# Optimization experiments

Measured on AMD Instinct MI355X. Metric: run time of the kernel, lower is better.

Reference implementation:

```python
import jax, jax.numpy as jnp
import numpy as np

N = 50000
E = 800000
IN_C, HID, OUT_C = 512, 256, 128


def gcn_conv(x, edge_index, W, b, num_nodes):
    # PyG GCNConv: add self-loops, symmetric normalization, linear-then-aggregate.
    h = x @ W  # [N, out]
    src = jnp.concatenate([edge_index[0], jnp.arange(num_nodes)])
    dst = jnp.concatenate([edge_index[1], jnp.arange(num_nodes)])
    ones = jnp.ones(src.shape[0], dtype=x.dtype)
    deg = jax.ops.segment_sum(ones, dst, num_segments=num_nodes)  # in-degree incl. self-loop
    dinv = jax.lax.rsqrt(deg)  # deg >= 1 thanks to self-loops
    norm = dinv[src] * dinv[dst]  # [E+N]
    msg = h[src] * norm[:, None]  # gather + scale
    out = jax.ops.segment_sum(msg, dst, num_segments=num_nodes)  # scatter-add
    return out + b


def setup_inputs() -> dict:
    key = jax.random.key(0)
    k_x, k_e, k_w1, k_b1, k_w2, k_b2 = jax.random.split(key, 6)
    x = jax.random.normal(k_x, (N, IN_C), dtype=jnp.float32)
    edge_index = jax.random.randint(k_e, (2, E), 0, N, dtype=jnp.int64)
    s1 = 1.0 / np.sqrt(IN_C)
    s2 = 1.0 / np.sqrt(HID)
    W1 = jax.random.uniform(k_w1, (IN_C, HID), jnp.float32, -s1, s1)
    b1 = jax.random.uniform(k_b1, (HID,), jnp.float32, -s1, s1)
    W2 = jax.random.uniform(k_w2, (HID, OUT_C), jnp.float32, -s2, s2)
    b2 = jax.random.uniform(k_b2, (OUT_C,), jnp.float32, -s2, s2)
    return {"x": x, "edge_index": edge_index, "W1": W1, "b1": b1, "W2": W2, "b2": b2}


def reference(x, edge_index, W1, b1, W2, b2):
    h = gcn_conv(x, edge_index, W1, b1, N)
    h = jax.nn.relu(h)
    # dropout in eval mode == identity
    return gcn_conv(h, edge_index, W2, b2, N)
```

## Files before the change

### kernel.cpp

```cpp
#include <hip/hip_runtime.h>
#include <stdint.h>

typedef __bf16 bf16_t;
typedef bf16_t bf16x8 __attribute__((ext_vector_type(8)));
typedef bf16_t bf16x4 __attribute__((ext_vector_type(4)));
typedef bf16_t bf16x2 __attribute__((ext_vector_type(2)));
typedef float  f32x4  __attribute__((ext_vector_type(4)));

#define IN_C 512
#define HID  256
#define OUTC 128

__global__ void k_detect(const void* __restrict__ ei, int* __restrict__ flag, int n_nodes) {
  if (blockIdx.x == 0 && threadIdx.x == 0) {
    const long long* p = (const long long*)ei;
    int ok = 1;
    for (int i = 0; i < 64; ++i) {
      long long v = p[i];
      if (v < 0 || v >= n_nodes) ok = 0;
    }
    *flag = ok;
  }
}

__global__ void k_decode_hist(const void* __restrict__ ei, const int* __restrict__ flag,
                              int* __restrict__ srcI, int* __restrict__ dstI,
                              int* __restrict__ cnt, int E) {
  int e = blockIdx.x * blockDim.x + threadIdx.x;
  if (e >= E) return;
  int s, d;
  if (*flag) {
    const long long* p = (const long long*)ei;
    s = (int)p[e];
    d = (int)p[(size_t)E + e];
  } else {
    const int* p = (const int*)ei;
    s = p[e];
    d = p[E + e];
  }
  srcI[e] = s;
  dstI[e] = d;
  atomicAdd(&cnt[d], 1);
}

__global__ void k_dinv(const int* __restrict__ cnt, float* __restrict__ dinv, int n) {
  int i = blockIdx.x * blockDim.x + threadIdx.x;
  if (i < n) dinv[i] = rsqrtf((float)cnt[i] + 1.0f);
}

__global__ void k_scan1(const int* __restrict__ cnt, int* __restrict__ ex,
                        int* __restrict__ part, int n) {
  __shared__ int sh[256];
  int i = blockIdx.x * 256 + threadIdx.x;
  int v = (i < n) ? cnt[i] : 0;
  sh[threadIdx.x] = v;
  __syncthreads();
  int val = v;
  for (int off = 1; off < 256; off <<= 1) {
    int t = (threadIdx.x >= off) ? sh[threadIdx.x - off] : 0;
    __syncthreads();
    val += t;
    sh[threadIdx.x] = val;
    __syncthreads();
  }
  if (i < n) ex[i] = val - v;
  if (threadIdx.x == 255) part[blockIdx.x] = val;
}

__global__ void k_scan2(int* __restrict__ part, int nb) {
  __shared__ int sh[256];
  int v = (threadIdx.x < nb) ? part[threadIdx.x] : 0;
  sh[threadIdx.x] = v;
  __syncthreads();
  int val = v;
  for (int off = 1; off < 256; off <<= 1) {
    int t = (threadIdx.x >= off) ? sh[threadIdx.x - off] : 0;
    __syncthreads();
    val += t;
    sh[threadIdx.x] = val;
    __syncthreads();
  }
  if (threadIdx.x < nb) part[threadIdx.x] = val - v;
}

__global__ void k_scan3(int* __restrict__ rs, const int* __restrict__ part,
                        int* __restrict__ cur, int n, int Etot) {
  int i = blockIdx.x * 256 + threadIdx.x;
  if (i < n) {
    int r = rs[i] + part[blockIdx.x];
    rs[i] = r;
    cur[i] = r;
  }
  if (i == 0) rs[n] = Etot;
}

__global__ void k_fill(const int* __restrict__ srcI, const int* __restrict__ dstI,
                       int* __restrict__ cur, int* __restrict__ csr, int E) {
  int e = blockIdx.x * blockDim.x + threadIdx.x;
  if (e >= E) return;
  int p = atomicAdd(&cur[dstI[e]], 1);
  csr[p] = srcI[e];
}

__global__ void k_convx(const float* __restrict__ x, bf16_t* __restrict__ Xb,
                        int n, int mpad) {
  int t = blockIdx.x * blockDim.x + threadIdx.x;
  int r = t >> 6, c8 = t & 63;
  if (r >= mpad) return;
  bf16x8 o;
  if (r < n) {
    const float4* px = (const float4*)(x + (size_t)r * IN_C);
    float4 a = px[c8 * 2];
    float4 b = px[c8 * 2 + 1];
    o[0] = (bf16_t)a.x; o[1] = (bf16_t)a.y; o[2] = (bf16_t)a.z; o[3] = (bf16_t)a.w;
    o[4] = (bf16_t)b.x; o[5] = (bf16_t)b.y; o[6] = (bf16_t)b.z; o[7] = (bf16_t)b.w;
  } else {
    for (int i = 0; i < 8; ++i) o[i] = (bf16_t)0.0f;
  }
  *(bf16x8*)(Xb + (size_t)r * IN_C + c8 * 8) = o;
}

__global__ void k_transpose(const float* __restrict__ W, bf16_t* __restrict__ Wt,
                            int K, int Ncols) {
  int t = blockIdx.x * blockDim.x + threadIdx.x;
  if (t >= K * Ncols) return;
  int k = t / Ncols, nn = t % Ncols;
  Wt[(size_t)nn * K + k] = (bf16_t)W[t];
}

__global__ __launch_bounds__(256, 2) void k_gemm(const bf16_t* __restrict__ A,
                                                 const bf16_t* __restrict__ Bt,
                                                 bf16_t* __restrict__ C,
                                                 int Kdim, int Ncols) {
  __shared__ bf16_t As[128 * 40];
  __shared__ bf16_t Bs[128 * 40];
  const int bm = blockIdx.x, bn = blockIdx.y;
  const int tid = threadIdx.x;
  const int wave = tid >> 6, lane = tid & 63;
  const int wm = (wave >> 1) * 64, wn = (wave & 1) * 64;
  const int quad = lane >> 4, l16 = lane & 15;
  const int seg = tid & 3;

  f32x4 acc[4][4];
  for (int i = 0; i < 4; ++i)
    for (int j = 0; j < 4; ++j)
      for (int r = 0; r < 4; ++r) acc[i][j][r] = 0.0f;

  for (int kk = 0; kk < Kdim; kk += 32) {
#pragma unroll
    for (int s = 0; s < 2; ++s) {
      int row = s * 64 + (tid >> 2);
      bf16x8 va = *(const bf16x8*)(A + (size_t)(bm * 128 + row) * Kdim + kk + seg * 8);
      *(bf16x8*)(&As[row * 40 + seg * 8]) = va;
      bf16x8 vb = *(const bf16x8*)(Bt + (size_t)(bn * 128 + row) * Kdim + kk + seg * 8);
      *(bf16x8*)(&Bs[row * 40 + seg * 8]) = vb;
    }
    __syncthreads();
    bf16x8 af[4], bfr[4];
#pragma unroll
    for (int i = 0; i < 4; ++i)
      af[i] = *(const bf16x8*)(&As[(wm + i * 16 + l16) * 40 + quad * 8]);
#pragma unroll
    for (int j = 0; j < 4; ++j)
      bfr[j] = *(const bf16x8*)(&Bs[(wn + j * 16 + l16) * 40 + quad * 8]);
#pragma unroll
    for (int i = 0; i < 4; ++i)
#pragma unroll
      for (int j = 0; j < 4; ++j)
        acc[i][j] = __builtin_amdgcn_mfma_f32_16x16x32_bf16(af[i], bfr[j], acc[i][j], 0, 0, 0);
    __syncthreads();
  }

#pragma unroll
  for (int i = 0; i < 4; ++i) {
#pragma unroll
    for (int j = 0; j < 4; ++j) {
      int col = bn * 128 + wn + j * 16 + l16;
      int row0 = bm * 128 + wm + i * 16 + quad * 4;
#pragma unroll
      for (int r = 0; r < 4; ++r)
        C[(size_t)(row0 + r) * Ncols + col] = (bf16_t)acc[i][j][r];
    }
  }
}

__global__ void k_agg_l1(const bf16_t* __restrict__ H, const int* __restrict__ rs,
                         const int* __restrict__ csr, const float* __restrict__ dinv,
                         const float* __restrict__ b1, bf16_t* __restrict__ R,
                         int n, int mpad) {
  int d = blockIdx.x * 4 + (threadIdx.x >> 6);
  if (d >= mpad) return;
  int lane = threadIdx.x & 63;
  if (d >= n) {
    bf16x4 z;
    z[0] = (bf16_t)0.0f; z[1] = (bf16_t)0.0f; z[2] = (bf16_t)0.0f; z[3] = (bf16_t)0.0f;
    *(bf16x4*)(R + (size_t)d * HID + lane * 4) = z;
    return;
  }
  int e0 = rs[d], e1 = rs[d + 1];
  float a0 = 0.f, a1 = 0.f, a2 = 0.f, a3 = 0.f;
  float c0 = 0.f, c1 = 0.f, c2 = 0.f, c3 = 0.f;
  int e = e0;
  for (; e + 2 <= e1; e += 2) {
    int s0 = csr[e], s1 = csr[e + 1];
    float w0 = dinv[s0], w1 = dinv[s1];
    bf16x4 h0 = *(const bf16x4*)(H + (size_t)s0 * HID + lane * 4);
    bf16x4 h1 = *(const bf16x4*)(H + (size_t)s1 * HID + lane * 4);
    a0 += w0 * (float)h0[0]; a1 += w0 * (float)h0[1];
    a2 += w0 * (float)h0[2]; a3 += w0 * (float)h0[3];
    c0 += w1 * (float)h1[0]; c1 += w1 * (float)h1[1];
    c2 += w1 * (float)h1[2]; c3 += w1 * (float)h1[3];
  }
  if (e < e1) {
    int s0 = csr[e];
    float w0 = dinv[s0];
    bf16x4 h0 = *(const bf16x4*)(H + (size_t)s0 * HID + lane * 4);
    a0 += w0 * (float)h0[0]; a1 += w0 * (float)h0[1];
    a2 += w0 * (float)h0[2]; a3 += w0 * (float)h0[3];
  }
  a0 += c0; a1 += c1; a2 += c2; a3 += c3;
  float dd = dinv[d];
  float dv2 = dd * dd;
  bf16x4 hs = *(const bf16x4*)(H + (size_t)d * HID + lane * 4);
  float4 bb = ((const float4*)b1)[lane];
  float v0 = fmaxf(a0 * dd + dv2 * (float)hs[0] + bb.x, 0.f);
  float v1 = fmaxf(a1 * dd + dv2 * (float)hs[1] + bb.y, 0.f);
  float v2 = fmaxf(a2 * dd + dv2 * (float)hs[2] + bb.z, 0.f);
  float v3 = fmaxf(a3 * dd + dv2 * (float)hs[3] + bb.w, 0.f);
  bf16x4 o;
  o[0] = (bf16_t)v0; o[1] = (bf16_t)v1; o[2] = (bf16_t)v2; o[3] = (bf16_t)v3;
  *(bf16x4*)(R + (size_t)d * HID + lane * 4) = o;
}

__global__ void k_agg_l2(const bf16_t* __restrict__ H, const int* __restrict__ rs,
                         const int* __restrict__ csr, const float* __restrict__ dinv,
                         const float* __restrict__ b2, float* __restrict__ out, int n) {
  int d = blockIdx.x * 4 + (threadIdx.x >> 6);
  if (d >= n) return;
  int lane = threadIdx.x & 63;
  int e0 = rs[d], e1 = rs[d + 1];
  float a0 = 0.f, a1 = 0.f, c0 = 0.f, c1 = 0.f;
  int e = e0;
  for (; e + 2 <= e1; e += 2) {
    int s0 = csr[e], s1 = csr[e + 1];
    float w0 = dinv[s0], w1 = dinv[s1];
    bf16x2 h0 = *(const bf16x2*)(H + (size_t)s0 * OUTC + lane * 2);
    bf16x2 h1 = *(const bf16x2*)(H + (size_t)s1 * OUTC + lane * 2);
    a0 += w0 * (float)h0[0]; a1 += w0 * (float)h0[1];
    c0 += w1 * (float)h1[0]; c1 += w1 * (float)h1[1];
  }
  if (e < e1) {
    int s0 = csr[e];
    float w0 = dinv[s0];
    bf16x2 h0 = *(const bf16x2*)(H + (size_t)s0 * OUTC + lane * 2);
    a0 += w0 * (float)h0[0]; a1 += w0 * (float)h0[1];
  }
  a0 += c0; a1 += c1;
  float dd = dinv[d];
  float dv2 = dd * dd;
  bf16x2 hs = *(const bf16x2*)(H + (size_t)d * OUTC + lane * 2);
  float2 bb = ((const float2*)b2)[lane];
  float2 o;
  o.x = a0 * dd + dv2 * (float)hs[0] + bb.x;
  o.y = a1 * dd + dv2 * (float)hs[1] + bb.y;
  ((float2*)(out + (size_t)d * OUTC))[lane] = o;
}

extern "C" void kernel_launch(void* const* d_in, const int* in_sizes, int n_in,
                              void* d_out, int out_size, void* d_ws, size_t ws_size,
                              hipStream_t stream) {
  const float* x  = (const float*)d_in[0];
  const void*  ei = d_in[1];
  const float* W1 = (const float*)d_in[2];
  const float* b1 = (const float*)d_in[3];
  const float* W2 = (const float*)d_in[4];
  const float* b2 = (const float*)d_in[5];

  const int n = in_sizes[0] / IN_C;
  const int E = in_sizes[1] / 2;
  const int mpad = (n + 127) & ~127;

  char* w = (char*)d_ws;
  size_t off = 0;
  auto alloc = [&](size_t bytes) -> void* {
    void* p = w + off;
    off = (off + bytes + 255) & ~(size_t)255;
    return p;
  };

  int*    flag = (int*)alloc(4);
  int*    srcI = (int*)alloc((size_t)E * 4);
  int*    dstI = (int*)alloc((size_t)E * 4);
  int*    cnt  = (int*)alloc((size_t)n * 4);
  float*  dinv = (float*)alloc((size_t)n * 4);
  int*    rs   = (int*)alloc((size_t)(n + 1) * 4);
  int*    cur  = (int*)alloc((size_t)n * 4);
  int*    part = (int*)alloc(1024);
  int*    csr  = (int*)alloc((size_t)E * 4);
  bf16_t* Xb   = (bf16_t*)alloc((size_t)mpad * IN_C * 2);
  bf16_t* W1t  = (bf16_t*)alloc((size_t)HID * IN_C * 2);
  bf16_t* H1b  = (bf16_t*)alloc((size_t)mpad * HID * 2);
  bf16_t* R1b  = (bf16_t*)alloc((size_t)mpad * HID * 2);
  bf16_t* W2t  = (bf16_t*)alloc((size_t)OUTC * HID * 2);
  bf16_t* H2b  = (bf16_t*)alloc((size_t)mpad * OUTC * 2);
  (void)ws_size; (void)n_in; (void)out_size;

  const int nb = (n + 255) / 256;

  hipMemsetAsync(cnt, 0, (size_t)n * 4, stream);
  k_detect<<<1, 64, 0, stream>>>(ei, flag, n);
  k_decode_hist<<<(E + 255) / 256, 256, 0, stream>>>(ei, flag, srcI, dstI, cnt, E);
  k_dinv<<<nb, 256, 0, stream>>>(cnt, dinv, n);
  k_scan1<<<nb, 256, 0, stream>>>(cnt, rs, part, n);
  k_scan2<<<1, 256, 0, stream>>>(part, nb);
  k_scan3<<<nb, 256, 0, stream>>>(rs, part, cur, n, E);
  k_fill<<<(E + 255) / 256, 256, 0, stream>>>(srcI, dstI, cur, csr, E);

  k_convx<<<(mpad * 64 + 255) / 256, 256, 0, stream>>>(x, Xb, n, mpad);
  k_transpose<<<(IN_C * HID + 255) / 256, 256, 0, stream>>>(W1, W1t, IN_C, HID);
  k_transpose<<<(HID * OUTC + 255) / 256, 256, 0, stream>>>(W2, W2t, HID, OUTC);

  k_gemm<<<dim3(mpad / 128, HID / 128), 256, 0, stream>>>(Xb, W1t, H1b, IN_C, HID);
  k_agg_l1<<<(mpad + 3) / 4, 256, 0, stream>>>(H1b, rs, csr, dinv, b1, R1b, n, mpad);
  k_gemm<<<dim3(mpad / 128, OUTC / 128), 256, 0, stream>>>(R1b, W2t, H2b, HID, OUTC);
  k_agg_l2<<<(n + 3) / 4, 256, 0, stream>>>(H2b, rs, csr, dinv, b2, (float*)d_out, n);
}
```

Before: 421.7 us.

## Fuse fp32-to-bf16 conversion into GEMM1, merge prep kernels, widen aggregation unroll

GEMM1 now reads fp32 x directly and converts to bf16 while staging tiles, which removes the separate conversion pass and the bf16 copy of x. The GEMM tiles change to 64 rows by the full output width, so GEMM1 uses one column block instead of two and each x tile is read once. Edge decode no longer writes int32 src/dst arrays: the histogram reads dst directly and the fill re-reads the raw edges, dinv is computed inside scan1, and the two weight transposes share one launch. The aggregation loops process four edges per step with independent accumulators to keep more gathers in flight, at the cost of more registers per thread.

```diff
diff --git a/kernel.cpp b/kernel.cpp
--- a/kernel.cpp
+++ b/kernel.cpp
@@ -23,9 +23,65 @@
   }
 }
 
-__global__ void k_decode_hist(const void* __restrict__ ei, const int* __restrict__ flag,
-                              int* __restrict__ srcI, int* __restrict__ dstI,
-                              int* __restrict__ cnt, int E) {
+__global__ void k_hist(const void* __restrict__ ei, const int* __restrict__ flag,
+                       int* __restrict__ cnt, int E) {
+  int e = blockIdx.x * blockDim.x + threadIdx.x;
+  if (e >= E) return;
+  int d;
+  if (*flag) d = (int)((const long long*)ei)[(size_t)E + e];
+  else       d = ((const int*)ei)[E + e];
+  atomicAdd(&cnt[d], 1);
+}
+
+__global__ void k_scan1(const int* __restrict__ cnt, int* __restrict__ ex,
+                        int* __restrict__ part, float* __restrict__ dinv, int n) {
+  __shared__ int sh[256];
+  int i = blockIdx.x * 256 + threadIdx.x;
+  int v = (i < n) ? cnt[i] : 0;
+  if (i < n) dinv[i] = rsqrtf((float)v + 1.0f);
+  sh[threadIdx.x] = v;
+  __syncthreads();
+  int val = v;
+  for (int off = 1; off < 256; off <<= 1) {
+    int t = (threadIdx.x >= off) ? sh[threadIdx.x - off] : 0;
+    __syncthreads();
+    val += t;
+    sh[threadIdx.x] = val;
+    __syncthreads();
+  }
+  if (i < n) ex[i] = val - v;
+  if (threadIdx.x == 255) part[blockIdx.x] = val;
+}
+
+__global__ void k_scan2(int* __restrict__ part, int nb) {
+  __shared__ int sh[256];
+  int v = (threadIdx.x < nb) ? part[threadIdx.x] : 0;
+  sh[threadIdx.x] = v;
+  __syncthreads();
+  int val = v;
+  for (int off = 1; off < 256; off <<= 1) {
+    int t = (threadIdx.x >= off) ? sh[threadIdx.x - off] : 0;
+    __syncthreads();
+    val += t;
+    sh[threadIdx.x] = val;
+    __syncthreads();
+  }
+  if (threadIdx.x < nb) part[threadIdx.x] = val - v;
+}
+
+__global__ void k_scan3(int* __restrict__ rs, const int* __restrict__ part,
+                        int* __restrict__ cur, int n, int Etot) {
+  int i = blockIdx.x * 256 + threadIdx.x;
+  if (i < n) {
+    int r = rs[i] + part[blockIdx.x];
+    rs[i] = r;
+    cur[i] = r;
+  }
+  if (i == 0) rs[n] = Etot;
+}
+
+__global__ void k_fill(const void* __restrict__ ei, const int* __restrict__ flag,
+                       int* __restrict__ cur, int* __restrict__ csr, int E) {
   int e = blockIdx.x * blockDim.x + threadIdx.x;
   if (e >= E) return;
   int s, d;
@@ -38,133 +94,124 @@
     s = p[e];
     d = p[E + e];
   }
-  srcI[e] = s;
-  dstI[e] = d;
-  atomicAdd(&cnt[d], 1);
-}
-
-__global__ void k_dinv(const int* __restrict__ cnt, float* __restrict__ dinv, int n) {
-  int i = blockIdx.x * blockDim.x + threadIdx.x;
-  if (i < n) dinv[i] = rsqrtf((float)cnt[i] + 1.0f);
-}
-
-__global__ void k_scan1(const int* __restrict__ cnt, int* __restrict__ ex,
-                        int* __restrict__ part, int n) {
-  __shared__ int sh[256];
-  int i = blockIdx.x * 256 + threadIdx.x;
-  int v = (i < n) ? cnt[i] : 0;
-  sh[threadIdx.x] = v;
-  __syncthreads();
-  int val = v;
-  for (int off = 1; off < 256; off <<= 1) {
-    int t = (threadIdx.x >= off) ? sh[threadIdx.x - off] : 0;
-    __syncthreads();
-    val += t;
-    sh[threadIdx.x] = val;
-    __syncthreads();
-  }
-  if (i < n) ex[i] = val - v;
-  if (threadIdx.x == 255) part[blockIdx.x] = val;
-}
-
-__global__ void k_scan2(int* __restrict__ part, int nb) {
-  __shared__ int sh[256];
-  int v = (threadIdx.x < nb) ? part[threadIdx.x] : 0;
-  sh[threadIdx.x] = v;
-  __syncthreads();
-  int val = v;
-  for (int off = 1; off < 256; off <<= 1) {
-    int t = (threadIdx.x >= off) ? sh[threadIdx.x - off] : 0;
-    __syncthreads();
-    val += t;
-    sh[threadIdx.x] = val;
-    __syncthreads();
-  }
-  if (threadIdx.x < nb) part[threadIdx.x] = val - v;
-}
-
-__global__ void k_scan3(int* __restrict__ rs, const int* __restrict__ part,
-                        int* __restrict__ cur, int n, int Etot) {
-  int i = blockIdx.x * 256 + threadIdx.x;
-  if (i < n) {
-    int r = rs[i] + part[blockIdx.x];
-    rs[i] = r;
-    cur[i] = r;
-  }
-  if (i == 0) rs[n] = Etot;
-}
-
-__global__ void k_fill(const int* __restrict__ srcI, const int* __restrict__ dstI,
-                       int* __restrict__ cur, int* __restrict__ csr, int E) {
-  int e = blockIdx.x * blockDim.x + threadIdx.x;
-  if (e >= E) return;
-  int p = atomicAdd(&cur[dstI[e]], 1);
-  csr[p] = srcI[e];
-}
-
-__global__ void k_convx(const float* __restrict__ x, bf16_t* __restrict__ Xb,
-                        int n, int mpad) {
+  int pos = atomicAdd(&cur[d], 1);
+  csr[pos] = s;
+}
+
+__global__ void k_transw(const float* __restrict__ W1, const float* __restrict__ W2,
+                         bf16_t* __restrict__ W1t, bf16_t* __restrict__ W2t) {
   int t = blockIdx.x * blockDim.x + threadIdx.x;
-  int r = t >> 6, c8 = t & 63;
-  if (r >= mpad) return;
-  bf16x8 o;
-  if (r < n) {
-    const float4* px = (const float4*)(x + (size_t)r * IN_C);
-    float4 a = px[c8 * 2];
-    float4 b = px[c8 * 2 + 1];
-    o[0] = (bf16_t)a.x; o[1] = (bf16_t)a.y; o[2] = (bf16_t)a.z; o[3] = (bf16_t)a.w;
-    o[4] = (bf16_t)b.x; o[5] = (bf16_t)b.y; o[6] = (bf16_t)b.z; o[7] = (bf16_t)b.w;
+  if (t < IN_C * HID) {
+    int k = t / HID, nn = t % HID;
+    W1t[(size_t)nn * IN_C + k] = (bf16_t)W1[t];
   } else {
-    for (int i = 0; i < 8; ++i) o[i] = (bf16_t)0.0f;
-  }
-  *(bf16x8*)(Xb + (size_t)r * IN_C + c8 * 8) = o;
-}
-
-__global__ void k_transpose(const float* __restrict__ W, bf16_t* __restrict__ Wt,
-                            int K, int Ncols) {
-  int t = blockIdx.x * blockDim.x + threadIdx.x;
-  if (t >= K * Ncols) return;
-  int k = t / Ncols, nn = t % Ncols;
-  Wt[(size_t)nn * K + k] = (bf16_t)W[t];
-}
-
-__global__ __launch_bounds__(256, 2) void k_gemm(const bf16_t* __restrict__ A,
-                                                 const bf16_t* __restrict__ Bt,
-                                                 bf16_t* __restrict__ C,
-                                                 int Kdim, int Ncols) {
-  __shared__ bf16_t As[128 * 40];
-  __shared__ bf16_t Bs[128 * 40];
-  const int bm = blockIdx.x, bn = blockIdx.y;
+    int u = t - IN_C * HID;
+    if (u < HID * OUTC) {
+      int k = u / OUTC, nn = u % OUTC;
+      W2t[(size_t)nn * HID + k] = (bf16_t)W2[u];
+    }
+  }
+}
+
+__global__ __launch_bounds__(256, 2) void k_gemm1(const float* __restrict__ x,
+                                                  const bf16_t* __restrict__ Bt,
+                                                  bf16_t* __restrict__ C, int n) {
+  __shared__ bf16_t As[64 * 40];
+  __shared__ bf16_t Bs[256 * 40];
+  const int bm = blockIdx.x;
   const int tid = threadIdx.x;
   const int wave = tid >> 6, lane = tid & 63;
-  const int wm = (wave >> 1) * 64, wn = (wave & 1) * 64;
+  const int wm = (wave >> 1) * 32, wn = (wave & 1) * 128;
   const int quad = lane >> 4, l16 = lane & 15;
-  const int seg = tid & 3;
-
-  f32x4 acc[4][4];
-  for (int i = 0; i < 4; ++i)
+  const int arow = tid >> 2, acol = (tid & 3) * 8;
+  const int grow = bm * 64 + arow;
+
+  f32x4 acc[2][8];
+  for (int i = 0; i < 2; ++i)
+    for (int j = 0; j < 8; ++j)
+      for (int r = 0; r < 4; ++r) acc[i][j][r] = 0.0f;
+
+  for (int kk = 0; kk < IN_C; kk += 32) {
+    bf16x8 va;
+    if (grow < n) {
+      const float4* px = (const float4*)(x + (size_t)grow * IN_C + kk + acol);
+      float4 a = px[0], b = px[1];
+      va[0] = (bf16_t)a.x; va[1] = (bf16_t)a.y; va[2] = (bf16_t)a.z; va[3] = (bf16_t)a.w;
+      va[4] = (bf16_t)b.x; va[5] = (bf16_t)b.y; va[6] = (bf16_t)b.z; va[7] = (bf16_t)b.w;
+    } else {
+      for (int i = 0; i < 8; ++i) va[i] = (bf16_t)0.0f;
+    }
+    *(bf16x8*)(&As[arow * 40 + acol]) = va;
+#pragma unroll
+    for (int c = 0; c < 4; ++c) {
+      bf16x8 vb = *(const bf16x8*)(Bt + (size_t)tid * IN_C + kk + c * 8);
+      *(bf16x8*)(&Bs[tid * 40 + c * 8]) = vb;
+    }
+    __syncthreads();
+    bf16x8 af[2], bfr[8];
+#pragma unroll
+    for (int i = 0; i < 2; ++i)
+      af[i] = *(const bf16x8*)(&As[(wm + i * 16 + l16) * 40 + quad * 8]);
+#pragma unroll
+    for (int j = 0; j < 8; ++j)
+      bfr[j] = *(const bf16x8*)(&Bs[(wn + j * 16 + l16) * 40 + quad * 8]);
+#pragma unroll
+    for (int i = 0; i < 2; ++i)
+#pragma unroll
+      for (int j = 0; j < 8; ++j)
+        acc[i][j] = __builtin_amdgcn_mfma_f32_16x16x32_bf16(af[i], bfr[j], acc[i][j], 0, 0, 0);
+    __syncthreads();
+  }
+
+#pragma unroll
+  for (int i = 0; i < 2; ++i) {
+#pragma unroll
+    for (int j = 0; j < 8; ++j) {
+      int col = wn + j * 16 + l16;
+      int row0 = bm * 64 + wm + i * 16 + quad * 4;
+#pragma unroll
+      for (int r = 0; r < 4; ++r)
+        C[(size_t)(row0 + r) * HID + col] = (bf16_t)acc[i][j][r];
+    }
+  }
+}
+
+__global__ __launch_bounds__(256, 2) void k_gemm2(const bf16_t* __restrict__ A,
+                                                  const bf16_t* __restrict__ Bt,
+                                                  bf16_t* __restrict__ C) {
+  __shared__ bf16_t As[64 * 40];
+  __shared__ bf16_t Bs[128 * 40];
+  const int bm = blockIdx.x;
+  const int tid = threadIdx.x;
+  const int wave = tid >> 6, lane = tid & 63;
+  const int wm = (wave >> 1) * 32, wn = (wave & 1) * 64;
+  const int quad = lane >> 4, l16 = lane & 15;
+  const int arow = tid >> 2, acol = (tid & 3) * 8;
+  const int brow = tid >> 1, bcol = (tid & 1) * 16;
+
+  f32x4 acc[2][4];
+  for (int i = 0; i < 2; ++i)
     for (int j = 0; j < 4; ++j)
       for (int r = 0; r < 4; ++r) acc[i][j][r] = 0.0f;
 
-  for (int kk = 0; kk < Kdim; kk += 32) {
-#pragma unroll
-    for (int s = 0; s < 2; ++s) {
-      int row = s * 64 + (tid >> 2);
-      bf16x8 va = *(const bf16x8*)(A + (size_t)(bm * 128 + row) * Kdim + kk + seg * 8);
-      *(bf16x8*)(&As[row * 40 + seg * 8]) = va;
-      bf16x8 vb = *(const bf16x8*)(Bt + (size_t)(bn * 128 + row) * Kdim + kk + seg * 8);
-      *(bf16x8*)(&Bs[row * 40 + seg * 8]) = vb;
-    }
-    __syncthreads();
-    bf16x8 af[4], bfr[4];
-#pragma unroll
-    for (int i = 0; i < 4; ++i)
+  for (int kk = 0; kk < HID; kk += 32) {
+    bf16x8 va = *(const bf16x8*)(A + (size_t)(bm * 64 + arow) * HID + kk + acol);
+    *(bf16x8*)(&As[arow * 40 + acol]) = va;
+#pragma unroll
+    for (int c = 0; c < 2; ++c) {
+      bf16x8 vb = *(const bf16x8*)(Bt + (size_t)brow * HID + kk + bcol + c * 8);
+      *(bf16x8*)(&Bs[brow * 40 + bcol + c * 8]) = vb;
+    }
+    __syncthreads();
+    bf16x8 af[2], bfr[4];
+#pragma unroll
+    for (int i = 0; i < 2; ++i)
       af[i] = *(const bf16x8*)(&As[(wm + i * 16 + l16) * 40 + quad * 8]);
 #pragma unroll
     for (int j = 0; j < 4; ++j)
       bfr[j] = *(const bf16x8*)(&Bs[(wn + j * 16 + l16) * 40 + quad * 8]);
 #pragma unroll
-    for (int i = 0; i < 4; ++i)
+    for (int i = 0; i < 2; ++i)
 #pragma unroll
       for (int j = 0; j < 4; ++j)
         acc[i][j] = __builtin_amdgcn_mfma_f32_16x16x32_bf16(af[i], bfr[j], acc[i][j], 0, 0, 0);
@@ -172,14 +219,14 @@
   }
 
 #pragma unroll
-  for (int i = 0; i < 4; ++i) {
+  for (int i = 0; i < 2; ++i) {
 #pragma unroll
     for (int j = 0; j < 4; ++j) {
-      int col = bn * 128 + wn + j * 16 + l16;
-      int row0 = bm * 128 + wm + i * 16 + quad * 4;
+      int col = wn + j * 16 + l16;
+      int row0 = bm * 64 + wm + i * 16 + quad * 4;
 #pragma unroll
       for (int r = 0; r < 4; ++r)
-        C[(size_t)(row0 + r) * Ncols + col] = (bf16_t)acc[i][j][r];
+        C[(size_t)(row0 + r) * OUTC + col] = (bf16_t)acc[i][j][r];
     }
   }
 }
@@ -198,31 +245,40 @@
     return;
   }
   int e0 = rs[d], e1 = rs[d + 1];
-  float a0 = 0.f, a1 = 0.f, a2 = 0.f, a3 = 0.f;
-  float c0 = 0.f, c1 = 0.f, c2 = 0.f, c3 = 0.f;
+  float acc[4][4];
+  for (int k = 0; k < 4; ++k)
+    for (int c = 0; c < 4; ++c) acc[k][c] = 0.f;
   int e = e0;
-  for (; e + 2 <= e1; e += 2) {
-    int s0 = csr[e], s1 = csr[e + 1];
-    float w0 = dinv[s0], w1 = dinv[s1];
+  for (; e + 4 <= e1; e += 4) {
+    int s0 = csr[e], s1 = csr[e + 1], s2 = csr[e + 2], s3 = csr[e + 3];
+    float w0 = dinv[s0], w1 = dinv[s1], w2 = dinv[s2], w3 = dinv[s3];
     bf16x4 h0 = *(const bf16x4*)(H + (size_t)s0 * HID + lane * 4);
     bf16x4 h1 = *(const bf16x4*)(H + (size_t)s1 * HID + lane * 4);
-    a0 += w0 * (float)h0[0]; a1 += w0 * (float)h0[1];
-    a2 += w0 * (float)h0[2]; a3 += w0 * (float)h0[3];
-    c0 += w1 * (float)h1[0]; c1 += w1 * (float)h1[1];
-    c2 += w1 * (float)h1[2]; c3 += w1 * (float)h1[3];
-  }
-  if (e < e1) {
+    bf16x4 h2 = *(const bf16x4*)(H + (size_t)s2 * HID + lane * 4);
+    bf16x4 h3 = *(const bf16x4*)(H + (size_t)s3 * HID + lane * 4);
+#pragma unroll
+    for (int c = 0; c < 4; ++c) {
+      acc[0][c] += w0 * (float)h0[c];
+      acc[1][c] += w1 * (float)h1[c];
+      acc[2][c] += w2 * (float)h2[c];
+      acc[3][c] += w3 * (float)h3[c];
+    }
+  }
+  for (; e < e1; ++e) {
     int s0 = csr[e];
     float w0 = dinv[s0];
     bf16x4 h0 = *(const bf16x4*)(H + (size_t)s0 * HID + lane * 4);
-    a0 += w0 * (float)h0[0]; a1 += w0 * (float)h0[1];
-    a2 += w0 * (float)h0[2]; a3 += w0 * (float)h0[3];
-  }
-  a0 += c0; a1 += c1; a2 += c2; a3 += c3;
+#pragma unroll
+    for (int c = 0; c < 4; ++c) acc[0][c] += w0 * (float)h0[c];
+  }
   float dd = dinv[d];
   float dv2 = dd * dd;
   bf16x4 hs = *(const bf16x4*)(H + (size_t)d * HID + lane * 4);
   float4 bb = ((const float4*)b1)[lane];
+  float a0 = acc[0][0] + acc[1][0] + acc[2][0] + acc[3][0];
+  float a1 = acc[0][1] + acc[1][1] + acc[2][1] + acc[3][1];
+  float a2 = acc[0][2] + acc[1][2] + acc[2][2] + acc[3][2];
+  float a3 = acc[0][3] + acc[1][3] + acc[2][3] + acc[3][3];
   float v0 = fmaxf(a0 * dd + dv2 * (float)hs[0] + bb.x, 0.f);
   float v1 = fmaxf(a1 * dd + dv2 * (float)hs[1] + bb.y, 0.f);
   float v2 = fmaxf(a2 * dd + dv2 * (float)hs[2] + bb.z, 0.f);
@@ -239,23 +295,29 @@
   if (d >= n) return;
   int lane = threadIdx.x & 63;
   int e0 = rs[d], e1 = rs[d + 1];
-  float a0 = 0.f, a1 = 0.f, c0 = 0.f, c1 = 0.f;
+  float acc[4][2];
+  for (int k = 0; k < 4; ++k) { acc[k][0] = 0.f; acc[k][1] = 0.f; }
   int e = e0;
-  for (; e + 2 <= e1; e += 2) {
-    int s0 = csr[e], s1 = csr[e + 1];
-    float w0 = dinv[s0], w1 = dinv[s1];
+  for (; e + 4 <= e1; e += 4) {
+    int s0 = csr[e], s1 = csr[e + 1], s2 = csr[e + 2], s3 = csr[e + 3];
+    float w0 = dinv[s0], w1 = dinv[s1], w2 = dinv[s2], w3 = dinv[s3];
     bf16x2 h0 = *(const bf16x2*)(H + (size_t)s0 * OUTC + lane * 2);
     bf16x2 h1 = *(const bf16x2*)(H + (size_t)s1 * OUTC + lane * 2);
-    a0 += w0 * (float)h0[0]; a1 += w0 * (float)h0[1];
-    c0 += w1 * (float)h1[0]; c1 += w1 * (float)h1[1];
-  }
-  if (e < e1) {
+    bf16x2 h2 = *(const bf16x2*)(H + (size_t)s2 * OUTC + lane * 2);
+    bf16x2 h3 = *(const bf16x2*)(H + (size_t)s3 * OUTC + lane * 2);
+    acc[0][0] += w0 * (float)h0[0]; acc[0][1] += w0 * (float)h0[1];
+    acc[1][0] += w1 * (float)h1[0]; acc[1][1] += w1 * (float)h1[1];
+    acc[2][0] += w2 * (float)h2[0]; acc[2][1] += w2 * (float)h2[1];
+    acc[3][0] += w3 * (float)h3[0]; acc[3][1] += w3 * (float)h3[1];
+  }
+  for (; e < e1; ++e) {
     int s0 = csr[e];
     float w0 = dinv[s0];
     bf16x2 h0 = *(const bf16x2*)(H + (size_t)s0 * OUTC + lane * 2);
-    a0 += w0 * (float)h0[0]; a1 += w0 * (float)h0[1];
-  }
-  a0 += c0; a1 += c1;
+    acc[0][0] += w0 * (float)h0[0]; acc[0][1] += w0 * (float)h0[1];
+  }
+  float a0 = acc[0][0] + acc[1][0] + acc[2][0] + acc[3][0];
+  float a1 = acc[0][1] + acc[1][1] + acc[2][1] + acc[3][1];
   float dd = dinv[d];
   float dv2 = dd * dd;
   bf16x2 hs = *(const bf16x2*)(H + (size_t)d * OUTC + lane * 2);
@@ -278,7 +340,7 @@
 
   const int n = in_sizes[0] / IN_C;
   const int E = in_sizes[1] / 2;
-  const int mpad = (n + 127) & ~127;
+  const int mpad = (n + 63) & ~63;
 
   char* w = (char*)d_ws;
   size_t off = 0;
@@ -289,19 +351,16 @@
   };
 
   int*    flag = (int*)alloc(4);
-  int*    srcI = (int*)alloc((size_t)E * 4);
-  int*    dstI = (int*)alloc((size_t)E * 4);
   int*    cnt  = (int*)alloc((size_t)n * 4);
   float*  dinv = (float*)alloc((size_t)n * 4);
   int*    rs   = (int*)alloc((size_t)(n + 1) * 4);
   int*    cur  = (int*)alloc((size_t)n * 4);
   int*    part = (int*)alloc(1024);
   int*    csr  = (int*)alloc((size_t)E * 4);
-  bf16_t* Xb   = (bf16_t*)alloc((size_t)mpad * IN_C * 2);
   bf16_t* W1t  = (bf16_t*)alloc((size_t)HID * IN_C * 2);
+  bf16_t* W2t  = (bf16_t*)alloc((size_t)OUTC * HID * 2);
   bf16_t* H1b  = (bf16_t*)alloc((size_t)mpad * HID * 2);
   bf16_t* R1b  = (bf16_t*)alloc((size_t)mpad * HID * 2);
-  bf16_t* W2t  = (bf16_t*)alloc((size_t)OUTC * HID * 2);
   bf16_t* H2b  = (bf16_t*)alloc((size_t)mpad * OUTC * 2);
   (void)ws_size; (void)n_in; (void)out_size;
 
@@ -309,19 +368,15 @@
 
   hipMemsetAsync(cnt, 0, (size_t)n * 4, stream);
   k_detect<<<1, 64, 0, stream>>>(ei, flag, n);
-  k_decode_hist<<<(E + 255) / 256, 256, 0, stream>>>(ei, flag, srcI, dstI, cnt, E);
-  k_dinv<<<nb, 256, 0, stream>>>(cnt, dinv, n);
-  k_scan1<<<nb, 256, 0, stream>>>(cnt, rs, part, n);
+  k_hist<<<(E + 255) / 256, 256, 0, stream>>>(ei, flag, cnt, E);
+  k_scan1<<<nb, 256, 0, stream>>>(cnt, rs, part, dinv, n);
   k_scan2<<<1, 256, 0, stream>>>(part, nb);
   k_scan3<<<nb, 256, 0, stream>>>(rs, part, cur, n, E);
-  k_fill<<<(E + 255) / 256, 256, 0, stream>>>(srcI, dstI, cur, csr, E);
-
-  k_convx<<<(mpad * 64 + 255) / 256, 256, 0, stream>>>(x, Xb, n, mpad);
-  k_transpose<<<(IN_C * HID + 255) / 256, 256, 0, stream>>>(W1, W1t, IN_C, HID);
-  k_transpose<<<(HID * OUTC + 255) / 256, 256, 0, stream>>>(W2, W2t, HID, OUTC);
-
-  k_gemm<<<dim3(mpad / 128, HID / 128), 256, 0, stream>>>(Xb, W1t, H1b, IN_C, HID);
+  k_fill<<<(E + 255) / 256, 256, 0, stream>>>(ei, flag, cur, csr, E);
+  k_transw<<<(IN_C * HID + HID * OUTC + 255) / 256, 256, 0, stream>>>(W1, W2, W1t, W2t);
+
+  k_gemm1<<<mpad / 64, 256, 0, stream>>>(x, W1t, H1b, n);
   k_agg_l1<<<(mpad + 3) / 4, 256, 0, stream>>>(H1b, rs, csr, dinv, b1, R1b, n, mpad);
-  k_gemm<<<dim3(mpad / 128, OUTC / 128), 256, 0, stream>>>(R1b, W2t, H2b, HID, OUTC);
+  k_gemm2<<<mpad / 64, 256, 0, stream>>>(R1b, W2t, H2b);
   k_agg_l2<<<(n + 3) / 4, 256, 0, stream>>>(H2b, rs, csr, dinv, b2, (float*)d_out, n);
 }
```

Measured after the change: 401.3 us. 4.8% less time.
